# Performance work log

Hardware: AMD Instinct MI355X
Metric: run time of the kernel (lower is better)

The kernel has to match this reference:

```python
import jax, jax.numpy as jnp
import numpy as np
import math

SEQ_LEN = 2048
DIM = 4096
N_HEADS = 32
N_KV_HEADS = 8
HEAD_DIM = DIM // N_HEADS  # 128
ROPE_THETA = 500000.0
W_SCALE = 0.02


def _precompute_freqs(head_dim, end, theta=ROPE_THETA):
    freq = 1.0 / theta ** (jnp.arange(0, head_dim, 2, dtype=jnp.float32) / head_dim)  # [hd/2]
    t = jnp.arange(end, dtype=jnp.float32)
    f = t[:, None] * freq[None, :]  # [S, hd/2]
    return jnp.cos(f), jnp.sin(f)


def _apply_rope(x, cos, sin):
    # x: [S, H, hd]; interleaved even/odd rotation, matching torch ::2 / 1::2 indexing
    xe = x[:, :, 0::2]
    xo = x[:, :, 1::2]
    c = cos[:, None, :]  # [S, 1, hd/2]
    s = sin[:, None, :]
    re = xe * c - xo * s
    ro = xe * s + xo * c
    # re-interleave: out[..., 2i] = re[..., i], out[..., 2i+1] = ro[..., i]
    return jnp.stack([re, ro], axis=-1).reshape(x.shape)


def setup_inputs() -> dict:
    key = jax.random.key(0)
    k = jax.random.split(key, 5)
    x = jax.random.normal(k[0], (SEQ_LEN, DIM), dtype=jnp.float32)
    wq = jax.random.normal(k[1], (DIM, DIM), dtype=jnp.float32) * W_SCALE
    wk = jax.random.normal(k[2], (N_KV_HEADS * HEAD_DIM, DIM), dtype=jnp.float32) * W_SCALE
    wv = jax.random.normal(k[3], (N_KV_HEADS * HEAD_DIM, DIM), dtype=jnp.float32) * W_SCALE
    wo = jax.random.normal(k[4], (DIM, DIM), dtype=jnp.float32) * W_SCALE
    return {"x": x, "wq": wq, "wk": wk, "wv": wv, "wo": wo}


def reference(x, wq, wk, wv, wo):
    S = SEQ_LEN
    rep = N_HEADS // N_KV_HEADS  # 4

    Q = (x @ wq.T).reshape(S, N_HEADS, HEAD_DIM)
    K = (x @ wk.T).reshape(S, N_KV_HEADS, HEAD_DIM)
    V = (x @ wv.T).reshape(S, N_KV_HEADS, HEAD_DIM)

    cos, sin = _precompute_freqs(HEAD_DIM, S)
    Q = _apply_rope(Q, cos, sin)
    K = _apply_rope(K, cos, sin)

    # GQA: repeat_interleave(K, rep, dim=1) maps query head h -> kv group h // rep.
    # Express natively with a grouped einsum instead of materializing repeated K/V.
    Qg = Q.transpose(1, 0, 2).reshape(N_KV_HEADS, rep, S, HEAD_DIM)  # [g, r, S, d]
    Kt = K.transpose(1, 0, 2)  # [g, S, d]
    Vt = V.transpose(1, 0, 2)  # [g, S, d]

    scores = jnp.einsum('grqd,gkd->grqk', Qg, Kt) / math.sqrt(HEAD_DIM)
    mask = jnp.triu(jnp.full((S, S), -jnp.inf, dtype=scores.dtype), k=1)
    probs = jax.nn.softmax(scores + mask, axis=-1)
    out = jnp.einsum('grqk,gkd->grqd', probs, Vt)  # [g, r, S, d]

    out = out.reshape(N_HEADS, S, HEAD_DIM).transpose(1, 0, 2).reshape(S, N_HEADS * HEAD_DIM)
    return out @ wo.T
```

## Files before the change

### kernel.cpp

```cpp
#include <hip/hip_runtime.h>

typedef unsigned short u16;
typedef short short8 __attribute__((ext_vector_type(8)));
typedef float f32x4 __attribute__((ext_vector_type(4)));
typedef unsigned short u16x4 __attribute__((ext_vector_type(4)));

typedef short8 short8_a __attribute__((may_alias));
typedef f32x4 f32x4_a __attribute__((may_alias));
typedef u16x4 u16x4_a __attribute__((may_alias));
typedef unsigned int uint_a __attribute__((may_alias));

__device__ __forceinline__ u16 f2b(float f) {
  unsigned u = __float_as_uint(f);
  u += 0x7FFFu + ((u >> 16) & 1u);
  return (u16)(u >> 16);
}

__device__ __forceinline__ void mfma_b(f32x4& d, short8 a, short8 b) {
  asm("v_mfma_f32_16x16x32_bf16 %0, %1, %2, %0" : "+v"(d) : "v"(a), "v"(b));
}

__device__ __forceinline__ void guard4(f32x4& a, f32x4& b, f32x4& c, f32x4& d) {
  asm volatile("s_nop 7\n\ts_nop 7" : "+v"(a), "+v"(b), "+v"(c), "+v"(d));
}
__device__ __forceinline__ void guard8(f32x4* o) {
  asm volatile("s_nop 7\n\ts_nop 7"
               : "+v"(o[0]), "+v"(o[1]), "+v"(o[2]), "+v"(o[3]),
                 "+v"(o[4]), "+v"(o[5]), "+v"(o[6]), "+v"(o[7]));
}

__device__ __forceinline__ void gload16(const void* g, void* l) {
  __builtin_amdgcn_global_load_lds((__attribute__((address_space(1))) void*)(g),
                                   (__attribute__((address_space(3))) void*)(l),
                                   16, 0, 0);
}

__device__ __forceinline__ void bar_v0() {
  asm volatile("s_waitcnt vmcnt(0)\n\ts_barrier" ::: "memory");
}
__device__ __forceinline__ void bar_v4() {
  asm volatile("s_waitcnt vmcnt(4)\n\ts_barrier" ::: "memory");
}

__global__ __launch_bounds__(256)
void k_prep(const float* __restrict__ x, const float* __restrict__ wq,
            const float* __restrict__ wk, const float* __restrict__ wv,
            const float* __restrict__ wo, u16* __restrict__ xb,
            u16* __restrict__ wB, u16* __restrict__ wob,
            float* __restrict__ cost, float* __restrict__ sint) {
  const long i = (long)blockIdx.x * 256 + threadIdx.x;
  const float* src;
  u16* dst;
  long j;
  if (i < 6291456) {
    if (i < 2097152) { src = x; dst = xb; j = i; }
    else { src = wq; dst = wB; j = i - 2097152; }
  } else if (i < 8388608) {
    if (i < 7340032) { src = wk; dst = wB + 16777216; j = i - 6291456; }
    else { src = wv; dst = wB + 20971520; j = i - 7340032; }
  } else if (i < 12582912) {
    src = wo; dst = wob; j = i - 8388608;
  } else {
    long ti = i - 12582912;
    int s = (int)(ti >> 6), jj = (int)(ti & 63);
    float freq = powf(500000.0f, -(float)jj * (1.0f / 64.0f));
    float a = (float)s * freq;
    float sv, cv;
    sincosf(a, &sv, &cv);
    cost[ti] = cv;
    sint[ti] = sv;
    return;
  }
  f32x4 v = ((const f32x4_a*)src)[j];
  u16x4 o;
  o[0] = f2b(v[0]); o[1] = f2b(v[1]); o[2] = f2b(v[2]); o[3] = f2b(v[3]);
  ((u16x4_a*)dst)[j] = o;
}

#define QK_SCALE 0.08838834764831845f
__global__ __launch_bounds__(512, 2)
void k_gemm8(const u16* __restrict__ A, const u16* __restrict__ B,
             const float* __restrict__ cost, const float* __restrict__ sint,
             u16* __restrict__ Qb, u16* __restrict__ Kb, u16* __restrict__ Vt) {
  extern __shared__ u16 lds[];
  const int K = 4096;
  const int tid = threadIdx.x;
  const int w = tid >> 6, lane = tid & 63;
  const int hi = lane >> 4, lo = lane & 15;
  const int wr = w >> 2, wc = w & 3;
  int bid = blockIdx.x;
  bid = (bid & 7) * 24 + (bid >> 3);
  const int tm = bid / 24, tn = bid - (bid / 24) * 24;
  const int m0 = tm << 8, n0 = tn << 8;

  const int kx = (((tid & 7) ^ ((tid >> 3) & 7)) << 3);
  const int r3 = tid >> 3;

  f32x4 acc[8][4] = {};
  short8 afr[4][2], bfr[4][2];

  const int sA0 = (wr * 128 + lo) * 64;
  const int sB0 = (wc * 64 + lo) * 64;
  const int sl0 = ((0 * 4 + hi) ^ (lo & 7)) * 8;
  const int sl1 = ((1 * 4 + hi) ^ (lo & 7)) * 8;

#define STAGE_A(sbuf, h, kt)                                                    \
  {                                                                             \
    _Pragma("unroll") for (int l = 0; l < 2; ++l) {                             \
      gload16(A + (long)(m0 + (h)*128 + l * 64 + r3) * K + (kt)*64 + kx,        \
              lds + (sbuf)*16384 + ((h)*128 + l * 64 + w * 8) * 64);            \
    }                                                                           \
  }
#define STAGE_B(sbuf, h, kt)                                                    \
  {                                                                             \
    _Pragma("unroll") for (int l = 0; l < 2; ++l) {                             \
      gload16(B + (long)(n0 + (h)*128 + l * 64 + r3) * K + (kt)*64 + kx,        \
              lds + 32768 + (sbuf)*16384 + ((h)*128 + l * 64 + w * 8) * 64);    \
    }                                                                           \
  }

  STAGE_A(0, 0, 0); STAGE_A(0, 1, 0);
  STAGE_B(0, 0, 0); STAGE_B(0, 1, 0);
  bar_v0();

  const int NI = K >> 7;
#define HALF_ITER(buf, stile, sbuf, dostage)                                    \
  {                                                                             \
    const u16* Ab_ = lds + (buf)*16384;                                         \
    const u16* Bb_ = lds + 32768 + (buf)*16384;                                 \
    if (dostage) { STAGE_A(sbuf, 0, stile); STAGE_A(sbuf, 1, stile); }          \
    _Pragma("unroll") for (int fn = 0; fn < 4; ++fn) {                          \
      bfr[fn][0] = *(const short8_a*)(Bb_ + sB0 + fn * 1024 + sl0);             \
      bfr[fn][1] = *(const short8_a*)(Bb_ + sB0 + fn * 1024 + sl1);             \
    }                                                                           \
    _Pragma("unroll") for (int fm = 0; fm < 4; ++fm) {                          \
      afr[fm][0] = *(const short8_a*)(Ab_ + sA0 + fm * 1024 + sl0);             \
      afr[fm][1] = *(const short8_a*)(Ab_ + sA0 + fm * 1024 + sl1);             \
    }                                                                           \
    __builtin_amdgcn_s_setprio(1);                                              \
    _Pragma("unroll") for (int fm = 0; fm < 4; ++fm)                            \
      _Pragma("unroll") for (int fn = 0; fn < 4; ++fn) {                        \
        mfma_b(acc[fm][fn], afr[fm][0], bfr[fn][0]);                            \
        mfma_b(acc[fm][fn], afr[fm][1], bfr[fn][1]);                            \
      }                                                                         \
    __builtin_amdgcn_s_setprio(0);                                              \
    if (dostage) { STAGE_B(sbuf, 0, stile); STAGE_B(sbuf, 1, stile); }          \
    _Pragma("unroll") for (int fm = 0; fm < 4; ++fm) {                          \
      afr[fm][0] = *(const short8_a*)(Ab_ + sA0 + (fm + 4) * 1024 + sl0);       \
      afr[fm][1] = *(const short8_a*)(Ab_ + sA0 + (fm + 4) * 1024 + sl1);       \
    }                                                                           \
    __builtin_amdgcn_s_setprio(1);                                              \
    _Pragma("unroll") for (int fm = 0; fm < 4; ++fm)                            \
      _Pragma("unroll") for (int fn = 0; fn < 4; ++fn) {                        \
        mfma_b(acc[fm + 4][fn], afr[fm][0], bfr[fn][0]);                        \
        mfma_b(acc[fm + 4][fn], afr[fm][1], bfr[fn][1]);                        \
      }                                                                         \
    __builtin_amdgcn_s_setprio(0);                                              \
    bar_v0();                                                                   \
  }

  for (int it = 0; it < NI; ++it) {
    HALF_ITER(0, 2 * it + 1, 1, true);
    HALF_ITER(1, 2 * it + 2, 0, (it + 1 < NI));
  }

  guard8(&acc[0][0]); guard8(&acc[2][0]); guard8(&acc[4][0]); guard8(&acc[6][0]);

  if (n0 < 5120) {
    const bool isQ = (n0 < 4096);
#pragma unroll
    for (int fm = 0; fm < 8; ++fm) {
      const int row0 = m0 + wr * 128 + fm * 16 + hi * 4;
#pragma unroll
      for (int fn = 0; fn < 4; ++fn) {
        const int c = n0 + wc * 64 + fn * 16 + lo;
        const int j0 = (c & 127) >> 1;
        const bool even = ((c & 1) == 0);
#pragma unroll
        for (int r = 0; r < 4; ++r) {
          float own = acc[fm][fn][r];
          float part = __shfl_xor(own, 1);
          const int s_ = row0 + r;
          const float cv = cost[s_ * 64 + j0];
          const float sv = sint[s_ * 64 + j0];
          float res = even ? (own * cv - part * sv) : (part * sv + own * cv);
          if (isQ)
            Qb[(long)s_ * 4096 + c] = f2b(res * QK_SCALE);
          else
            Kb[(long)s_ * 1024 + (c - 4096)] = f2b(res);
        }
      }
    }
  } else {
#pragma unroll
    for (int fm = 0; fm < 8; ++fm) {
      const int row0 = m0 + wr * 128 + fm * 16 + hi * 4;
#pragma unroll
      for (int fn = 0; fn < 4; ++fn) {
        const int vc = n0 - 5120 + wc * 64 + fn * 16 + lo;
        u16x4 pk;
#pragma unroll
        for (int r = 0; r < 4; ++r) pk[r] = f2b(acc[fm][fn][r]);
        *(u16x4_a*)(Vt + (long)vc * 2048 + row0) = pk;
      }
    }
  }
#undef HALF_ITER
#undef STAGE_A
#undef STAGE_B
}

template <int EPI>
__global__ __launch_bounds__(256, 2)
void k_gemm_t(const u16* __restrict__ A, const u16* __restrict__ B,
              float* __restrict__ C, int M, int N, int K) {
  __shared__ u16 As[12288];
  __shared__ u16 Bs[12288];
  const int tid = threadIdx.x;
  const int w = tid >> 6, lane = tid & 63;
  const int hi = lane >> 4, lo = lane & 15;
  const int nwg = gridDim.x;
  int bid = blockIdx.x;
  if ((nwg & 7) == 0) bid = (bid & 7) * (nwg >> 3) + (bid >> 3);
  const int ntn = N >> 7;
  const int tm = bid / ntn, tn = bid - tm * ntn;
  const int m0 = tm << 7, n0 = tn << 7;
  const int wr = w >> 1, wc = w & 1;

  const int rowl = w * 16 + (lane >> 2);
  const int ks = (((lane & 3) ^ ((lane >> 3) & 3)) << 3);
  const u16* Ag0 = A + (long)(m0 + rowl) * K + ks;
  const u16* Ag1 = A + (long)(m0 + 64 + rowl) * K + ks;
  const u16* Bg0 = B + (long)(n0 + rowl) * K + ks;
  const u16* Bg1 = B + (long)(n0 + 64 + rowl) * K + ks;
  const int sb = w * 512;

  f32x4 acc[4][4] = {};
  const int hs = hi ^ ((lo >> 1) & 3);
  const int aoff = (wr * 64 + lo) * 32 + hs * 8;
  const int boff = (wc * 64 + lo) * 32 + hs * 8;

  const int nt = K >> 5;
  int c0 = 0, c1 = 4096, c2 = 8192;

  gload16(Ag0, As + c0 + sb);       gload16(Ag1, As + c0 + sb + 2048);
  gload16(Bg0, Bs + c0 + sb);       gload16(Bg1, Bs + c0 + sb + 2048);
  gload16(Ag0 + 32, As + c1 + sb);  gload16(Ag1 + 32, As + c1 + sb + 2048);
  gload16(Bg0 + 32, Bs + c1 + sb);  gload16(Bg1 + 32, Bs + c1 + sb + 2048);
  bar_v4();

  for (int t = 0; t < nt; ++t) {
    if (t + 2 < nt) {
      const int k0 = (t + 2) << 5;
      gload16(Ag0 + k0, As + c2 + sb);
      gload16(Ag1 + k0, As + c2 + sb + 2048);
      gload16(Bg0 + k0, Bs + c2 + sb);
      gload16(Bg1 + k0, Bs + c2 + sb + 2048);
    }
    short8 af[4], bf[4];
#pragma unroll
    for (int m = 0; m < 4; ++m)
      af[m] = *(const short8_a*)(As + c0 + aoff + m * 512);
#pragma unroll
    for (int n = 0; n < 4; ++n)
      bf[n] = *(const short8_a*)(Bs + c0 + boff + n * 512);
    __builtin_amdgcn_s_setprio(1);
#pragma unroll
    for (int m = 0; m < 4; ++m)
#pragma unroll
      for (int n = 0; n < 4; ++n) mfma_b(acc[m][n], af[m], bf[n]);
    __builtin_amdgcn_s_setprio(0);
    if (t + 2 < nt) bar_v4();
    else bar_v0();
    const int tmp = c0; c0 = c1; c1 = c2; c2 = tmp;
  }
  guard8(&acc[0][0]);
  guard8(&acc[2][0]);

#pragma unroll
  for (int m = 0; m < 4; ++m) {
    const int row0 = m0 + wr * 64 + m * 16 + hi * 4;
#pragma unroll
    for (int n = 0; n < 4; ++n) {
      const int col = n0 + wc * 64 + n * 16 + lo;
#pragma unroll
      for (int r = 0; r < 4; ++r)
        C[(long)(row0 + r) * N + col] = acc[m][n][r];
    }
  }
}

#define KLD 136
#define VLD 72
__global__ __launch_bounds__(256, 2)
void k_attn(const u16* __restrict__ Qb, const u16* __restrict__ Kb,
            const u16* __restrict__ Vt, u16* __restrict__ Ab) {
  __shared__ u16 Ks[64 * KLD];
  __shared__ u16 Vs[128 * VLD];
  __shared__ u16 Ps[4 * 16 * VLD];

  const int tid = threadIdx.x;
  const int w = tid >> 6, lane = tid & 63;
  const int hi = lane >> 4, lo = lane & 15;
  const int qt = 31 - (blockIdx.x >> 5);
  const int h = blockIdx.x & 31;
  const int hkv = h >> 2;
  const int q0 = qt * 64;
  const int qrow = q0 + w * 16 + lo;

  short8 qf[4];
#pragma unroll
  for (int c = 0; c < 4; ++c)
    qf[c] = *(const short8_a*)(Qb + (long)qrow * 4096 + h * 128 + c * 32 + hi * 8);

  f32x4 o[8] = {};
  float m_run = -1e30f, l_run = 0.f;
  u16* Pw = Ps + w * (16 * VLD);

  const int ntiles = qt + 1;
  for (int t = 0; t < ntiles; ++t) {
    const int kv0 = t * 64;
    __syncthreads();
#pragma unroll
    for (int r = 0; r < 4; ++r) {
      int i = r * 256 + tid;
      int key = i >> 4, d8 = (i & 15) * 8;
      short8 v = *(const short8_a*)(Kb + (long)(kv0 + key) * 1024 + hkv * 128 + d8);
      *(short8_a*)(Ks + key * KLD + d8) = v;
    }
#pragma unroll
    for (int r = 0; r < 4; ++r) {
      int i = r * 256 + tid;
      int dd = i >> 3, k8 = (i & 7) * 8;
      short8 v = *(const short8_a*)(Vt + (long)hkv * 262144 + (long)dd * 2048 + kv0 + k8);
      *(short8_a*)(Vs + dd * VLD + k8) = v;
    }
    __syncthreads();

    f32x4 sc[4] = {};
#pragma unroll
    for (int c = 0; c < 4; ++c) {
#pragma unroll
      for (int kt = 0; kt < 4; ++kt) {
        short8 kf = *(const short8_a*)(Ks + (kt * 16 + lo) * KLD + c * 32 + hi * 8);
        mfma_b(sc[kt], kf, qf[c]);
      }
    }
    guard4(sc[0], sc[1], sc[2], sc[3]);

    if (t == ntiles - 1) {
#pragma unroll
      for (int kt = 0; kt < 4; ++kt)
#pragma unroll
        for (int r = 0; r < 4; ++r) {
          int key = kv0 + kt * 16 + hi * 4 + r;
          if (key > qrow) sc[kt][r] = -1e30f;
        }
    }
    float tmax = -1e30f;
#pragma unroll
    for (int kt = 0; kt < 4; ++kt)
#pragma unroll
      for (int r = 0; r < 4; ++r) tmax = fmaxf(tmax, sc[kt][r]);
    tmax = fmaxf(tmax, __shfl_xor(tmax, 16));
    tmax = fmaxf(tmax, __shfl_xor(tmax, 32));
    float m_new = fmaxf(m_run, tmax);
    float scale = __expf(m_run - m_new);
    float psum = 0.f;
    float p[16];
#pragma unroll
    for (int kt = 0; kt < 4; ++kt)
#pragma unroll
      for (int r = 0; r < 4; ++r) {
        float pv = __expf(sc[kt][r] - m_new);
        p[kt * 4 + r] = pv;
        psum += pv;
      }
    psum += __shfl_xor(psum, 16);
    psum += __shfl_xor(psum, 32);
    l_run = l_run * scale + psum;
    m_run = m_new;
    float srow[4];
#pragma unroll
    for (int r = 0; r < 4; ++r) srow[r] = __shfl(scale, hi * 4 + r);
#pragma unroll
    for (int n = 0; n < 8; ++n)
#pragma unroll
      for (int r = 0; r < 4; ++r) o[n][r] *= srow[r];
#pragma unroll
    for (int kt = 0; kt < 4; ++kt) {
      unsigned p01 = (unsigned)f2b(p[kt * 4]) | ((unsigned)f2b(p[kt * 4 + 1]) << 16);
      unsigned p23 = (unsigned)f2b(p[kt * 4 + 2]) | ((unsigned)f2b(p[kt * 4 + 3]) << 16);
      *(uint_a*)(Pw + lo * VLD + kt * 16 + hi * 4) = p01;
      *(uint_a*)(Pw + lo * VLD + kt * 16 + hi * 4 + 2) = p23;
    }
    __syncthreads();
#pragma unroll
    for (int c = 0; c < 2; ++c) {
      short8 pf = *(const short8_a*)(Pw + lo * VLD + c * 32 + hi * 8);
#pragma unroll
      for (int n = 0; n < 8; ++n) {
        short8 vf = *(const short8_a*)(Vs + (n * 16 + lo) * VLD + c * 32 + hi * 8);
        mfma_b(o[n], pf, vf);
      }
    }
  }
  guard8(o);

  float inv = 1.0f / l_run;
  float irow[4];
#pragma unroll
  for (int r = 0; r < 4; ++r) irow[r] = __shfl(inv, hi * 4 + r);
#pragma unroll
  for (int n = 0; n < 8; ++n)
#pragma unroll
    for (int r = 0; r < 4; ++r) {
      int q = q0 + w * 16 + hi * 4 + r;
      Ab[(long)q * 4096 + h * 128 + n * 16 + lo] = f2b(o[n][r] * irow[r]);
    }
}

extern "C" void kernel_launch(void* const* d_in, const int* in_sizes, int n_in,
                              void* d_out, int out_size, void* d_ws, size_t ws_size,
                              hipStream_t stream) {
  const float* x = (const float*)d_in[0];
  const float* wq = (const float*)d_in[1];
  const float* wk = (const float*)d_in[2];
  const float* wv = (const float*)d_in[3];
  const float* wo = (const float*)d_in[4];
  float* out = (float*)d_out;
  char* ws = (char*)d_ws;

  size_t off = 0;
  u16* xb = (u16*)(ws + off); off += 16777216;
  u16* wB = (u16*)(ws + off); off += 50331648;
  u16* wob = (u16*)(ws + off); off += 33554432;
  u16* Qb = (u16*)(ws + off); off += 16777216;
  u16* Kb = (u16*)(ws + off); off += 4194304;
  u16* Vtb = (u16*)(ws + off); off += 4194304;
  float* cost = (float*)(ws + off); off += 524288;
  float* sint = (float*)(ws + off); off += 524288;
  u16* Ab = (u16*)(ws + off); off += 16777216;

  static bool attr_set = false;
  if (!attr_set) {
    hipFuncSetAttribute((const void*)k_gemm8,
                        hipFuncAttributeMaxDynamicSharedMemorySize, 131072);
    attr_set = true;
  }

  k_prep<<<49664, 256, 0, stream>>>(x, wq, wk, wv, wo, xb, wB, wob, cost, sint);

  k_gemm8<<<192, 512, 131072, stream>>>(xb, wB, cost, sint, Qb, Kb, Vtb);

  k_attn<<<1024, 256, 0, stream>>>(Qb, Kb, Vtb, Ab);

  k_gemm_t<0><<<512, 256, 0, stream>>>(Ab, wob, out, 2048, 4096, 4096);
}
```

Measured before the change: 371.2 us.

## Widen output projection GEMM tile to 128x256 with 512-thread blocks

Replaces the 128x128-tile, 256-thread output projection GEMM with a specialized 128x256-tile kernel using 8 waves. Each block now reuses its A tile across twice as many columns, which halves the A-tile global loads per output and halves the grid to 256 blocks. Triple-buffered LDS grows to 72KB of dynamic shared memory. The larger block and LDS footprint may limit occupancy, and the grid now matches the CU count, which can leave some CUs idle.

After: 350.6 us (median of 2 runs). -5.5%, faster.

```diff
diff --git a/kernel.cpp b/kernel.cpp
--- a/kernel.cpp
+++ b/kernel.cpp
@@ -38,8 +38,8 @@
 __device__ __forceinline__ void bar_v0() {
   asm volatile("s_waitcnt vmcnt(0)\n\ts_barrier" ::: "memory");
 }
-__device__ __forceinline__ void bar_v4() {
-  asm volatile("s_waitcnt vmcnt(4)\n\ts_barrier" ::: "memory");
+__device__ __forceinline__ void bar_v3() {
+  asm volatile("s_waitcnt vmcnt(3)\n\ts_barrier" ::: "memory");
 }
 
 __global__ __launch_bounds__(256)
@@ -210,29 +210,27 @@
 #undef STAGE_B
 }
 
-template <int EPI>
-__global__ __launch_bounds__(256, 2)
-void k_gemm_t(const u16* __restrict__ A, const u16* __restrict__ B,
-              float* __restrict__ C, int M, int N, int K) {
-  __shared__ u16 As[12288];
-  __shared__ u16 Bs[12288];
+__global__ __launch_bounds__(512, 2)
+void k_gemm_t2(const u16* __restrict__ A, const u16* __restrict__ B,
+               float* __restrict__ C) {
+  extern __shared__ u16 lds2[];
+  u16* As = lds2;
+  u16* Bs = lds2 + 12288;
+  const int K = 4096, N = 4096;
   const int tid = threadIdx.x;
   const int w = tid >> 6, lane = tid & 63;
   const int hi = lane >> 4, lo = lane & 15;
-  const int nwg = gridDim.x;
+  const int wr = w >> 2, wc = w & 3;
   int bid = blockIdx.x;
-  if ((nwg & 7) == 0) bid = (bid & 7) * (nwg >> 3) + (bid >> 3);
-  const int ntn = N >> 7;
-  const int tm = bid / ntn, tn = bid - tm * ntn;
-  const int m0 = tm << 7, n0 = tn << 7;
-  const int wr = w >> 1, wc = w & 1;
-
-  const int rowl = w * 16 + (lane >> 2);
-  const int ks = (((lane & 3) ^ ((lane >> 3) & 3)) << 3);
-  const u16* Ag0 = A + (long)(m0 + rowl) * K + ks;
-  const u16* Ag1 = A + (long)(m0 + 64 + rowl) * K + ks;
-  const u16* Bg0 = B + (long)(n0 + rowl) * K + ks;
-  const u16* Bg1 = B + (long)(n0 + 64 + rowl) * K + ks;
+  bid = (bid & 7) * 32 + (bid >> 3);
+  const int tm = bid >> 4, tn = bid & 15;
+  const int m0 = tm << 7, n0 = tn << 8;
+
+  const int r2 = tid >> 2;
+  const int ks = (((tid & 3) ^ ((tid >> 3) & 3)) << 3);
+  const u16* Ag = A + (long)(m0 + r2) * K + ks;
+  const u16* Bg0 = B + (long)(n0 + r2) * K + ks;
+  const u16* Bg1 = B + (long)(n0 + 128 + r2) * K + ks;
   const int sb = w * 512;
 
   f32x4 acc[4][4] = {};
@@ -241,39 +239,39 @@
   const int boff = (wc * 64 + lo) * 32 + hs * 8;
 
   const int nt = K >> 5;
-  int c0 = 0, c1 = 4096, c2 = 8192;
-
-  gload16(Ag0, As + c0 + sb);       gload16(Ag1, As + c0 + sb + 2048);
-  gload16(Bg0, Bs + c0 + sb);       gload16(Bg1, Bs + c0 + sb + 2048);
-  gload16(Ag0 + 32, As + c1 + sb);  gload16(Ag1 + 32, As + c1 + sb + 2048);
-  gload16(Bg0 + 32, Bs + c1 + sb);  gload16(Bg1 + 32, Bs + c1 + sb + 2048);
-  bar_v4();
+  int i0 = 0, i1 = 1, i2 = 2;
+
+#define STG2(kt, bi)                                      \
+  {                                                       \
+    gload16(Ag + (kt)*32, As + (bi)*4096 + sb);           \
+    gload16(Bg0 + (kt)*32, Bs + (bi)*8192 + sb);          \
+    gload16(Bg1 + (kt)*32, Bs + (bi)*8192 + 4096 + sb);   \
+  }
+
+  STG2(0, 0);
+  STG2(1, 1);
+  bar_v3();
 
   for (int t = 0; t < nt; ++t) {
-    if (t + 2 < nt) {
-      const int k0 = (t + 2) << 5;
-      gload16(Ag0 + k0, As + c2 + sb);
-      gload16(Ag1 + k0, As + c2 + sb + 2048);
-      gload16(Bg0 + k0, Bs + c2 + sb);
-      gload16(Bg1 + k0, Bs + c2 + sb + 2048);
-    }
+    if (t + 2 < nt) STG2(t + 2, i2);
     short8 af[4], bf[4];
 #pragma unroll
     for (int m = 0; m < 4; ++m)
-      af[m] = *(const short8_a*)(As + c0 + aoff + m * 512);
+      af[m] = *(const short8_a*)(As + i0 * 4096 + aoff + m * 512);
 #pragma unroll
     for (int n = 0; n < 4; ++n)
-      bf[n] = *(const short8_a*)(Bs + c0 + boff + n * 512);
+      bf[n] = *(const short8_a*)(Bs + i0 * 8192 + boff + n * 512);
     __builtin_amdgcn_s_setprio(1);
 #pragma unroll
     for (int m = 0; m < 4; ++m)
 #pragma unroll
       for (int n = 0; n < 4; ++n) mfma_b(acc[m][n], af[m], bf[n]);
     __builtin_amdgcn_s_setprio(0);
-    if (t + 2 < nt) bar_v4();
+    if (t + 2 < nt) bar_v3();
     else bar_v0();
-    const int tmp = c0; c0 = c1; c1 = c2; c2 = tmp;
-  }
+    const int tmp = i0; i0 = i1; i1 = i2; i2 = tmp;
+  }
+#undef STG2
   guard8(&acc[0][0]);
   guard8(&acc[2][0]);
 
@@ -446,6 +444,8 @@
   if (!attr_set) {
     hipFuncSetAttribute((const void*)k_gemm8,
                         hipFuncAttributeMaxDynamicSharedMemorySize, 131072);
+    hipFuncSetAttribute((const void*)k_gemm_t2,
+                        hipFuncAttributeMaxDynamicSharedMemorySize, 73728);
     attr_set = true;
   }
 
@@ -455,5 +455,5 @@
 
   k_attn<<<1024, 256, 0, stream>>>(Qb, Kb, Vtb, Ab);
 
-  k_gemm_t<0><<<512, 256, 0, stream>>>(Ab, wob, out, 2048, 4096, 4096);
-}
+  k_gemm_t2<<<256, 512, 73728, stream>>>(Ab, wob, out);
+}
```
